# Kernel tuning notes

Measured on AMD Instinct MI355X. Metric: run time of the kernel, lower is better.

The kernel has to match this reference:

```python
import jax, jax.numpy as jnp
import numpy as np

B, L, D, T = 2, 2048, 1536, 2
INITRANGE = 0.1

def setup_inputs() -> dict:
    key = jax.random.key(0)
    k1, k2 = jax.random.split(key)
    hidden_states = jax.random.normal(k1, (B, L, D), dtype=jnp.float32)
    # decoder: Linear(2*D, T) with uniform(-0.1, 0.1) weight, zero bias
    W = jax.random.uniform(k2, (T, 2 * D), dtype=jnp.float32, minval=-INITRANGE, maxval=INITRANGE)
    b = jnp.zeros((T,), dtype=jnp.float32)
    return {"hidden_states": hidden_states, "W": W, "b": b}

def reference(hidden_states, W, b):
    # Faithful fused version of:
    #   prod = h[:,:,None,:] * h[:,None,:,:]; diff = h[:,:,None,:] - h[:,None,:,:]
    #   logits = cat(prod, diff, -1) @ W.T + b
    # Split W into the product half and the difference half.
    d = hidden_states.shape[-1]
    Wp, Wd = W[:, :d], W[:, d:]                      # [T, D] each
    # prod term: sum_d h[b,i,d] * h[b,j,d] * Wp[t,d]
    hw = jnp.einsum('bid,td->btid', hidden_states, Wp)          # [B,T,L,D]
    prod_logits = jnp.einsum('btid,bjd->bijt', hw, hidden_states)  # [B,L,L,T]
    # diff term: (h[b,i]-h[b,j]) @ Wd.T = (h@Wd.T)[b,i] - (h@Wd.T)[b,j]
    hd = jnp.einsum('bid,td->bit', hidden_states, Wd)           # [B,L,T]
    diff_logits = hd[:, :, None, :] - hd[:, None, :, :]         # [B,L,L,T]
    logits = prod_logits + diff_logits + b
    # symmetrize over the (i, j) pair axes
    logits = (logits + jnp.transpose(logits, (0, 2, 1, 3))) * 0.5
    return logits
```

## Files before the change

### kernel.cpp

```cpp
#include <hip/hip_runtime.h>
#include <hip/hip_bf16.h>
#include <stdint.h>

#define B_ 2
#define L_ 2048
#define D_ 1536

typedef __attribute__((ext_vector_type(4))) float  f32x4;
typedef __attribute__((ext_vector_type(8))) __bf16 bf16x8;

__device__ __forceinline__ unsigned short f2bf(float f) {
  unsigned int u = __float_as_uint(f);
  u += 0x7fffu + ((u >> 16) & 1u);
  return (unsigned short)(u >> 16);
}

__global__ __launch_bounds__(256) void conv_kernel(
    const float* __restrict__ hs, const float* __restrict__ W,
    unsigned short* __restrict__ X, unsigned short* __restrict__ P) {
  const int idx  = blockIdx.x * 256 + threadIdx.x;
  const int base = idx * 4;
  const int d    = base % D_;
  const float4 h  = *(const float4*)(hs + base);
  const float4 w0 = *(const float4*)(W + d);
  const float4 w1 = *(const float4*)(W + 2 * D_ + d);
  ushort4 x, p0, p1;
  x.x  = f2bf(h.x);        x.y  = f2bf(h.y);        x.z  = f2bf(h.z);        x.w  = f2bf(h.w);
  p0.x = f2bf(h.x * w0.x); p0.y = f2bf(h.y * w0.y); p0.z = f2bf(h.z * w0.z); p0.w = f2bf(h.w * w0.w);
  p1.x = f2bf(h.x * w1.x); p1.y = f2bf(h.y * w1.y); p1.z = f2bf(h.z * w1.z); p1.w = f2bf(h.w * w1.w);
  *(ushort4*)(X + base) = x;
  *(ushort4*)(P + base) = p0;
  *(ushort4*)(P + (size_t)B_ * L_ * D_ + base) = p1;
}

__device__ __forceinline__ void gload16(const unsigned short* g, unsigned short* l) {
  __builtin_amdgcn_global_load_lds(
      (const __attribute__((address_space(1))) unsigned int*)g,
      (__attribute__((address_space(3))) unsigned int*)l, 16, 0, 0);
}

__global__ __launch_bounds__(512, 2) void gemm_kernel(
    const unsigned short* __restrict__ X, const unsigned short* __restrict__ P,
    const float* __restrict__ bias, float2* __restrict__ out) {
  __shared__ unsigned short lds[65536];

  const int tid = threadIdx.x;

  const int id  = blockIdx.x;
  const int swz = (id & 7) * 32 + (id >> 3);
  const int bz  = swz >> 7;
  const int t2  = swz & 127;
  const int I0  = (t2 >> 3) * 128;
  const int J0  = (t2 & 7) * 256;

  const size_t planeB = (size_t)B_ * L_ * D_;

  const size_t gsrcOff = (size_t)(tid >> 2) * D_ +
                         (size_t)((((tid & 3) ^ ((tid >> 3) & 3))) * 8);
  const unsigned short* sA0 = P + (size_t)(bz * L_ + I0) * D_ + gsrcOff;
  const unsigned short* sA1 = sA0 + planeB;
  const unsigned short* sB0 = X + (size_t)(bz * L_ + J0) * D_ + gsrcOff;
  const unsigned short* sB1 = sB0 + (size_t)128 * D_;
  const int wuni = (tid >> 6) * 512;

  const int lane = tid & 63;
  const int w    = tid >> 6;
  const int wr   = w & 1;
  const int wc   = w >> 1;
  const int lr   = lane & 15;
  const int q    = lane >> 4;
  const int slot8 = ((q ^ ((lr >> 1) & 3)) * 8);
  int aOff[8], bOff[4];
#pragma unroll
  for (int m = 0; m < 8; ++m)
    aOff[m] = (m >> 2) * 4096 + (wr * 64 + (m & 3) * 16 + lr) * 32;
#pragma unroll
  for (int n = 0; n < 4; ++n)
    bOff[n] = 8192 + (n >> 1) * 4096 + (wc * 32 + (n & 1) * 16 + lr) * 32;

  f32x4  acc[8][4] = {};
  bf16x8 aF[8], bF[4];

#define STG4(NB, KH, KTN)                                                     \
  do {                                                                        \
    const size_t ko = (size_t)((KTN) * 64 + (KH) * 32);                       \
    gload16(sA0 + ko, lds + (NB) + (KH) * 16384 + 0     + wuni);              \
    gload16(sA1 + ko, lds + (NB) + (KH) * 16384 + 4096  + wuni);              \
    gload16(sB0 + ko, lds + (NB) + (KH) * 16384 + 8192  + wuni);              \
    gload16(sB1 + ko, lds + (NB) + (KH) * 16384 + 12288 + wuni);              \
  } while (0)

#define RDALL(CB, KH)                                                         \
  do {                                                                        \
    const unsigned short* base_ = lds + (CB) + (KH) * 16384 + slot8;          \
    _Pragma("unroll") for (int m = 0; m < 8; ++m)                             \
      aF[m] = *(const bf16x8*)(base_ + aOff[m]);                              \
    _Pragma("unroll") for (int n = 0; n < 4; ++n)                             \
      bF[n] = *(const bf16x8*)(base_ + bOff[n]);                              \
  } while (0)

#define MMALL()                                                               \
  do {                                                                        \
    _Pragma("unroll") for (int m = 0; m < 8; ++m)                             \
      _Pragma("unroll") for (int n = 0; n < 4; ++n)                           \
        acc[m][n] = __builtin_amdgcn_mfma_f32_16x16x32_bf16(                  \
            aF[m], bF[n], acc[m][n], 0, 0, 0);                                \
  } while (0)

#define BAR()   __builtin_amdgcn_s_barrier()
#define LGKM0() asm volatile("s_waitcnt lgkmcnt(0)" ::: "memory")
#define WVM(n)  asm volatile("s_waitcnt vmcnt(" #n ")" ::: "memory")
#define PRIO1() __builtin_amdgcn_s_setprio(1)
#define PRIO0() __builtin_amdgcn_s_setprio(0)

#define KSTEP(CB, NB, KTN)                                                    \
  do {                                                                        \
                                                                \
    RDALL(CB, 0); STG4(NB, 0, KTN);                                           \
    BAR(); LGKM0();                                                           \
    PRIO1(); MMALL(); PRIO0();                                                \
    WVM(4); BAR();                                                            \
                                                                \
    RDALL(CB, 1); STG4(NB, 1, KTN);                                           \
    BAR(); LGKM0();                                                           \
    PRIO1(); MMALL(); PRIO0();                                                \
    WVM(4); BAR();                                                            \
  } while (0)

#define KTAIL(CB)                                                             \
  do {                                                                        \
    RDALL(CB, 0);                                                             \
    BAR(); LGKM0();                                                           \
    PRIO1(); MMALL(); PRIO0();                                                \
    WVM(0); BAR();                                                            \
    RDALL(CB, 1);                                                             \
    LGKM0();                                                                  \
    PRIO1(); MMALL(); PRIO0();                                                \
  } while (0)

  STG4(0, 0, 0);
  STG4(0, 1, 0);
  WVM(4); BAR();

#pragma unroll 1
  for (int it = 0; it < 11; ++it) {
    const int kt0 = 2 * it;
    KSTEP(0,     32768, kt0 + 1);
    KSTEP(32768, 0,     kt0 + 2);
  }
  KSTEP(0, 32768, 23);
  KTAIL(32768);

#undef KSTEP
#undef KTAIL
#undef STG4
#undef RDALL
#undef MMALL

  const float bias0 = bias[0], bias1 = bias[1];
#pragma unroll
  for (int m = 0; m < 4; ++m) {
#pragma unroll
    for (int r = 0; r < 4; ++r) {
      const int i = I0 + wr * 64 + m * 16 + q * 4 + r;
      float2* orow = out + (size_t)(bz * L_ + i) * L_;
#pragma unroll
      for (int n = 0; n < 4; ++n) {
        const int j = J0 + (n >> 1) * 128 + wc * 32 + (n & 1) * 16 + lr;
        float2 v;
        v.x = acc[m][n][r] + bias0;
        v.y = acc[m + 4][n][r] + bias1;
        orow[j] = v;
      }
    }
  }
}

extern "C" void kernel_launch(void* const* d_in, const int* in_sizes, int n_in,
                              void* d_out, int out_size, void* d_ws, size_t ws_size,
                              hipStream_t stream) {
  const float* hs   = (const float*)d_in[0];
  const float* W    = (const float*)d_in[1];
  const float* bias = (const float*)d_in[2];

  unsigned short* X = (unsigned short*)d_ws;
  unsigned short* P = X + (size_t)B_ * L_ * D_;

  const int nconv = (B_ * L_ * D_ / 4) / 256;
  conv_kernel<<<nconv, 256, 0, stream>>>(hs, W, X, P);

  gemm_kernel<<<256, 512, 0, stream>>>(X, P, bias, (float2*)d_out);
}
```

Baseline: 139.9 us.

## Restructure GEMM K-loop into four-buffer LDS ring with one barrier per two phases

The bf16 MFMA GEMM main loop now splits LDS into four 32-wide K buffers in a ring instead of two double-buffered 64-wide stages with half-steps. Each phase reads one buffer and issues async global-to-LDS loads two phases ahead. A single vmcnt(0)+barrier boundary now covers every two phases, replacing the several barriers and lgkm waits per step used before. The aim is less synchronisation overhead. In exchange, the full vmcnt drain at each boundary may expose load latency, and there is no explicit lgkmcnt wait before the MFMAs.

```diff
diff --git a/kernel.cpp b/kernel.cpp
--- a/kernel.cpp
+++ b/kernel.cpp
@@ -38,6 +38,11 @@
       (const __attribute__((address_space(1))) unsigned int*)g,
       (__attribute__((address_space(3))) unsigned int*)l, 16, 0, 0);
 }
+
+#define B0O 0
+#define B1O 16384
+#define B2O 32768
+#define B3O 49152
 
 __global__ __launch_bounds__(512, 2) void gemm_kernel(
     const unsigned short* __restrict__ X, const unsigned short* __restrict__ P,
@@ -81,18 +86,18 @@
   f32x4  acc[8][4] = {};
   bf16x8 aF[8], bF[4];
 
-#define STG4(NB, KH, KTN)                                                     \
+#define STG4(NB, PN)                                                          \
   do {                                                                        \
-    const size_t ko = (size_t)((KTN) * 64 + (KH) * 32);                       \
-    gload16(sA0 + ko, lds + (NB) + (KH) * 16384 + 0     + wuni);              \
-    gload16(sA1 + ko, lds + (NB) + (KH) * 16384 + 4096  + wuni);              \
-    gload16(sB0 + ko, lds + (NB) + (KH) * 16384 + 8192  + wuni);              \
-    gload16(sB1 + ko, lds + (NB) + (KH) * 16384 + 12288 + wuni);              \
+    const size_t ko = (size_t)((PN) * 32);                                    \
+    gload16(sA0 + ko, lds + (NB) + 0     + wuni);                             \
+    gload16(sA1 + ko, lds + (NB) + 4096  + wuni);                             \
+    gload16(sB0 + ko, lds + (NB) + 8192  + wuni);                             \
+    gload16(sB1 + ko, lds + (NB) + 12288 + wuni);                             \
   } while (0)
 
-#define RDALL(CB, KH)                                                         \
+#define RDALL(CB)                                                             \
   do {                                                                        \
-    const unsigned short* base_ = lds + (CB) + (KH) * 16384 + slot8;          \
+    const unsigned short* base_ = lds + (CB) + slot8;                         \
     _Pragma("unroll") for (int m = 0; m < 8; ++m)                             \
       aF[m] = *(const bf16x8*)(base_ + aOff[m]);                              \
     _Pragma("unroll") for (int n = 0; n < 4; ++n)                             \
@@ -107,52 +112,52 @@
             aF[m], bF[n], acc[m][n], 0, 0, 0);                                \
   } while (0)
 
-#define BAR()   __builtin_amdgcn_s_barrier()
-#define LGKM0() asm volatile("s_waitcnt lgkmcnt(0)" ::: "memory")
-#define WVM(n)  asm volatile("s_waitcnt vmcnt(" #n ")" ::: "memory")
+#define BNDRY()                                                               \
+  do {                                                                        \
+    asm volatile("s_waitcnt vmcnt(0)" ::: "memory");                          \
+    __builtin_amdgcn_s_barrier();                                             \
+    __builtin_amdgcn_sched_barrier(0);                                        \
+  } while (0)
+
 #define PRIO1() __builtin_amdgcn_s_setprio(1)
 #define PRIO0() __builtin_amdgcn_s_setprio(0)
 
-#define KSTEP(CB, NB, KTN)                                                    \
+#define PH(CB, SB, PN)                                                        \
   do {                                                                        \
-                                                                \
-    RDALL(CB, 0); STG4(NB, 0, KTN);                                           \
-    BAR(); LGKM0();                                                           \
-    PRIO1(); MMALL(); PRIO0();                                                \
-    WVM(4); BAR();                                                            \
-                                                                \
-    RDALL(CB, 1); STG4(NB, 1, KTN);                                           \
-    BAR(); LGKM0();                                                           \
-    PRIO1(); MMALL(); PRIO0();                                                \
-    WVM(4); BAR();                                                            \
-  } while (0)
-
-#define KTAIL(CB)                                                             \
-  do {                                                                        \
-    RDALL(CB, 0);                                                             \
-    BAR(); LGKM0();                                                           \
-    PRIO1(); MMALL(); PRIO0();                                                \
-    WVM(0); BAR();                                                            \
-    RDALL(CB, 1);                                                             \
-    LGKM0();                                                                  \
+    RDALL(CB); STG4(SB, (PN) + 2);                                            \
     PRIO1(); MMALL(); PRIO0();                                                \
   } while (0)
 
-  STG4(0, 0, 0);
-  STG4(0, 1, 0);
-  WVM(4); BAR();
+#define PHNS(CB)                                                              \
+  do {                                                                        \
+    RDALL(CB);                                                                \
+    PRIO1(); MMALL(); PRIO0();                                                \
+  } while (0)
+
+  STG4(B0O, 0);
+  STG4(B1O, 1);
 
 #pragma unroll 1
   for (int it = 0; it < 11; ++it) {
-    const int kt0 = 2 * it;
-    KSTEP(0,     32768, kt0 + 1);
-    KSTEP(32768, 0,     kt0 + 2);
+    const int p0 = 4 * it;
+    BNDRY();
+    PH(B0O, B2O, p0);
+    PH(B1O, B3O, p0 + 1);
+    BNDRY();
+    PH(B2O, B0O, p0 + 2);
+    PH(B3O, B1O, p0 + 3);
   }
-  KSTEP(0, 32768, 23);
-  KTAIL(32768);
 
-#undef KSTEP
-#undef KTAIL
+  BNDRY();
+  PH(B0O, B2O, 44);
+  PH(B1O, B3O, 45);
+  BNDRY();
+  PHNS(B2O);
+  PHNS(B3O);
+
+#undef PH
+#undef PHNS
+#undef BNDRY
 #undef STG4
 #undef RDALL
 #undef MMALL
```

Measured after the change: 136.5 us. 2.5% less time.
